# Optimization experiments

Hardware: AMD Instinct MI355X
Metric: run time of the kernel (lower is better)

The kernel has to match this reference:

```python
import jax, jax.numpy as jnp
import numpy as np

SR = 24000          # sample_rate
HOP = 256           # hop_length
K = 1024            # FIR kernel_size = nearest_power_of_two(2.2/50*24000)
RC = 512            # rnn_channels
NF = 4              # n_formants
REV = 24000         # reverb length in samples
L = HOP + K - 1     # per-frame conv output length = 1279
PI = np.pi


def _gru(x, W_ih, W_hh, b_ih, b_hh):
    # x: [B, T, H] -> [B, T, H], torch nn.GRU semantics, h0 = 0
    B = x.shape[0]

    def step(h, xt):
        gi = xt @ W_ih.T + b_ih
        gh = h @ W_hh.T + b_hh
        i_r, i_z, i_n = jnp.split(gi, 3, axis=-1)
        h_r, h_z, h_n = jnp.split(gh, 3, axis=-1)
        r = jax.nn.sigmoid(i_r + h_r)
        zg = jax.nn.sigmoid(i_z + h_z)
        n = jnp.tanh(i_n + r * h_n)
        h = (1.0 - zg) * n + zg * h
        return h, h

    h0 = jnp.zeros((B, RC), x.dtype)
    _, ys = jax.lax.scan(step, h0, jnp.swapaxes(x, 0, 1))
    return jnp.swapaxes(ys, 0, 1)


def setup_inputs() -> dict:
    key = jax.random.key(0)
    ks = jax.random.split(key, 20)
    B, F = 4, 2048
    s = 0.05
    inp = {
        'f0': jax.random.uniform(ks[0], (B, F, 1), minval=100.0, maxval=300.0),
        'loudness': jax.random.normal(ks[1], (B, F, 1)),
        'gender': jax.random.uniform(ks[2], (B, F, 2)),
        'age': jax.random.uniform(ks[3], (B, F, 8)),
        'z': jax.random.normal(ks[4], (B, F, 16)),
        'noise': jax.random.normal(ks[5], (B, F, HOP)),
        'W_in': jax.random.normal(ks[6], (RC, 28)) * s, 'b_in': jnp.zeros((RC,)),
        'W_ih': jax.random.normal(ks[7], (3 * RC, RC)) * s,
        'W_hh': jax.random.normal(ks[8], (3 * RC, RC)) * s,
        'b_ih': jnp.zeros((3 * RC,)), 'b_hh': jnp.zeros((3 * RC,)),
        'W_oq': jax.random.normal(ks[9], (1, RC)) * s, 'b_oq': jnp.zeros((1,)),
        'W_vg': jax.random.normal(ks[10], (1, RC)) * s, 'b_vg': jnp.zeros((1,)),
        'W_ug': jax.random.normal(ks[11], (1, RC)) * s, 'b_ug': jnp.zeros((1,)),
        'W_ff': jax.random.normal(ks[12], (NF, RC)) * s, 'b_ff': jnp.zeros((NF,)),
        'W_fb': jax.random.normal(ks[13], (NF, RC)) * s, 'b_fb': jnp.zeros((NF,)),
        'reverb_ir': jax.random.normal(ks[14], (REV,)) * jnp.exp(-jnp.linspace(0.0, 5.0, REV)),
        'wet_logit': jnp.float32(-1.5),
    }
    return inp


def reference(f0, loudness, gender, age, z, noise,
              W_in, b_in, W_ih, W_hh, b_ih, b_hh,
              W_oq, b_oq, W_vg, b_vg, W_ug, b_ug,
              W_ff, b_ff, W_fb, b_fb, reverb_ir, wet_logit):
    B, F, _ = f0.shape

    # ---- controller ----
    f0c = f0 - jnp.mean(f0, axis=1, keepdims=True)
    inputs = jnp.concatenate([f0c, loudness, gender, age, z], axis=-1)  # [B,F,28]
    x = jax.nn.relu(inputs @ W_in.T + b_in)
    x = _gru(x, W_ih, W_hh, b_ih, b_hh)                                  # [B,F,512]
    oq = jax.nn.sigmoid(x @ W_oq.T + b_oq)                               # [B,F,1]
    v_gain = jax.nn.softplus(x @ W_vg.T + b_vg)
    u_gain = jax.nn.softplus(x @ W_ug.T + b_ug)
    ff = jnp.cumsum(jax.nn.softplus(x @ W_ff.T + b_ff), axis=-1) + 200.0  # [B,F,4]
    fb = jax.nn.softplus(x @ W_fb.T + b_fb) + 50.0

    # ---- Rosenberg glottal source ----
    cycles = f0 * (HOP / SR)                       # [B,F,1]
    cum = jnp.cumsum(cycles, axis=1)
    start = cum - cycles
    start = start - jnp.floor(start)
    ramp = (jnp.arange(HOP, dtype=f0.dtype) / SR)[None, None, :]
    total = start + f0 * ramp                      # [B,F,HOP]
    phi = total - jnp.floor(total)
    eps = 1e-6
    peak = oq * 0.66
    rise = 0.5 * (1.0 - jnp.cos(PI * phi / (peak + eps)))
    fall = jnp.cos(PI * (phi - peak) / (2.0 * (oq - peak) + eps))
    voiced = jnp.where(phi < peak, rise, 0.0)
    voiced = jnp.where((phi >= peak) & (phi < oq), fall, voiced)

    # ---- excitation ----
    excitation = voiced * v_gain + noise * u_gain   # [B,F,HOP]

    # ---- time-varying FIR formant filter ----
    t = jnp.arange(K, dtype=f0.dtype) / SR          # [K]
    ir = jnp.exp(-PI * fb[..., None] * t) * jnp.sin(2.0 * PI * ff[..., None] * t)  # [B,F,4,K]
    combined = jnp.sum(ir, axis=2)                  # [B,F,K]
    scale = jnp.max(jnp.abs(combined), axis=-1, keepdims=True) + 1e-8
    filt = combined / scale
    # torch conv1d is cross-correlation with padding K-1 == full convolution with flipped kernel
    NFFT = 2048  # >= L = 1279, power of two
    Xf = jnp.fft.rfft(excitation, n=NFFT)
    Hf = jnp.fft.rfft(filt[..., ::-1], n=NFFT)
    conv = jnp.fft.irfft(Xf * Hf, n=NFFT)[..., :L]  # [B,F,L]

    # ---- overlap-add (F.fold) ----
    total_len = (F - 1) * HOP + L
    idx = (jnp.arange(F)[:, None] * HOP + jnp.arange(L)[None, :]).reshape(-1)
    audio = jnp.zeros((B, total_len), conv.dtype).at[:, idx].add(conv.reshape(B, -1))

    # ---- FFT reverb ----
    FFTN = 1 << 20  # >= total_len + REV - 1 = 549310
    Af = jnp.fft.rfft(audio, n=FFTN)
    Rf = jnp.fft.rfft(reverb_ir, n=FFTN)
    wetsig = jnp.fft.irfft(Af * Rf[None, :], n=FFTN)[:, :total_len]
    wet = jax.nn.sigmoid(wet_logit)
    out = ((1.0 - wet) * audio + wet * wetsig)[..., None]  # [B,total_len,1]

    return out, oq, v_gain, u_gain, ff, fb
```

## Files before the change

kernel.cpp:

```cpp
#include <hip/hip_runtime.h>
#include <hip/hip_bf16.h>
#include <math.h>

#define PI_F 3.14159265358979323846f
#define TWO_PI_F 6.283185307179586f

constexpr int BB = 4;
constexpr int FF_ = 2048;
constexpr int RC = 512;
constexpr int HOP = 256;
constexpr int KK = 1024;
constexpr int LL = HOP + KK - 1;
constexpr size_t TOT = 525311;
constexpr int APAD = 24064;
constexpr size_t AROW = 549376;
constexpr int REV = 24000;
constexpr size_t AROW2 = 551424;

constexpr size_t O1 = 2101244;
constexpr size_t O2 = 2109436;
constexpr size_t O3 = 2117628;
constexpr size_t O4 = 2125820;
constexpr size_t O5 = 2158588;

constexpr size_t OFF_X      = 0;
constexpr size_t OFF_GI     = 16777216;
constexpr size_t OFF_HS     = 67108864;
constexpr size_t OFF_OQ     = 83886080;
constexpr size_t OFF_VG     = 83918848;
constexpr size_t OFF_UG     = 83951616;
constexpr size_t OFF_FFW    = 83984384;
constexpr size_t OFF_FBW    = 84115456;
constexpr size_t OFF_START  = 84246528;
constexpr size_t OFF_F0M    = 84279296;
constexpr size_t OFF_WTAP   = 50331648;
constexpr size_t OFF_AUDIO  = 92684800;
constexpr size_t OFF_AF16   = OFF_X;

constexpr size_t OFF_HBUF   = OFF_FFW;

__device__ __forceinline__ float softplusf(float x) {
  return x > 20.0f ? x : log1pf(expf(x));
}
__device__ __forceinline__ float sigmoidf_(float x) {
  return 1.0f / (1.0f + expf(-x));
}
__device__ __forceinline__ float fastrcp(float x) {
#if __has_builtin(__builtin_amdgcn_rcpf)
  return __builtin_amdgcn_rcpf(x);
#else
  return 1.0f / x;
#endif
}

typedef _Float16 half2v __attribute__((ext_vector_type(2)));
typedef _Float16 f16x8 __attribute__((ext_vector_type(8)));
typedef float f32x4 __attribute__((ext_vector_type(4)));

__device__ __forceinline__ float dot2f(unsigned wa, unsigned hb, float acc) {
#if __has_builtin(__builtin_amdgcn_fdot2)
  union { unsigned u; half2v h; } A, B;
  A.u = wa; B.u = hb;
  return __builtin_amdgcn_fdot2(A.h, B.h, acc, false);
#else
  union { unsigned u; _Float16 h[2]; } A, B;
  A.u = wa; B.u = hb;
  return fmaf((float)A.h[0], (float)B.h[0], fmaf((float)A.h[1], (float)B.h[1], acc));
#endif
}

__global__ __launch_bounds__(256) void k_f0mean(const float* __restrict__ f0, float* __restrict__ f0m) {
  int b = blockIdx.x, tid = threadIdx.x;
  float s = 0.f;
  for (int t = tid; t < FF_; t += 256) s += f0[b*FF_ + t];
  #pragma unroll
  for (int m = 1; m < 64; m <<= 1) s += __shfl_xor(s, m);
  __shared__ float ws4[4];
  if ((tid & 63) == 0) ws4[tid >> 6] = s;
  __syncthreads();
  if (tid == 0) f0m[b] = (ws4[0] + ws4[1] + ws4[2] + ws4[3]) * (1.0f / 2048.0f);
}

__global__ __launch_bounds__(256) void k_inproj(
    const float* __restrict__ f0, const float* __restrict__ loud,
    const float* __restrict__ gender, const float* __restrict__ age,
    const float* __restrict__ z, const float* __restrict__ f0m,
    const float* __restrict__ Win, const float* __restrict__ bin,
    float* __restrict__ x)
{
  __shared__ float inp[16 * 28];
  int r0 = blockIdx.x * 16;
  int tid = threadIdx.x;
  for (int i = tid; i < 16 * 28; i += 256) {
    int r = i / 28, c = i % 28;
    int bf = r0 + r, b = bf >> 11;
    float v;
    if (c == 0)       v = f0[bf] - f0m[b];
    else if (c == 1)  v = loud[bf];
    else if (c < 4)   v = gender[(size_t)bf*2 + (c - 2)];
    else if (c < 12)  v = age[(size_t)bf*8 + (c - 4)];
    else              v = z[(size_t)bf*16 + (c - 12)];
    inp[i] = v;
  }
  __syncthreads();
  for (int o = tid; o < 16 * 512; o += 256) {
    int r = o >> 9, j = o & 511;
    const float* w = Win + j * 28;
    const float* ip = inp + r * 28;
    float a = bin[j];
    #pragma unroll
    for (int c2 = 0; c2 < 28; ++c2) a = fmaf(w[c2], ip[c2], a);
    x[(size_t)(r0 + r) * 512 + j] = fmaxf(a, 0.0f);
  }
}

__global__ __launch_bounds__(256) void k_gemm_gi(
    const float* __restrict__ A, const float* __restrict__ Bw,
    const float* __restrict__ bias, float* __restrict__ C)
{
  __shared__ unsigned As[64 * 20];
  __shared__ unsigned Bs[64 * 20];
  int tid = threadIdx.x;
  int n0 = blockIdx.x * 64, m0 = blockIdx.y * 64;
  const int w = tid >> 6;
  const int lane = tid & 63;
  const int mrow0 = (w >> 1) * 32;
  const int ncol0 = (w & 1) * 32;
  const int lm = lane & 15;
  const int quad = lane >> 4;

  f32x4 acc00 = {0.f,0.f,0.f,0.f}, acc01 = {0.f,0.f,0.f,0.f};
  f32x4 acc10 = {0.f,0.f,0.f,0.f}, acc11 = {0.f,0.f,0.f,0.f};

  for (int k0 = 0; k0 < 512; k0 += 32) {
    __syncthreads();
    for (int i = tid; i < 1024; i += 256) {
      int r = i >> 4, d = i & 15;
      float2 av = *(const float2*)(A + (size_t)(m0 + r) * 512 + k0 + 2 * d);
      float2 bv = *(const float2*)(Bw + (size_t)(n0 + r) * 512 + k0 + 2 * d);
      union { unsigned u32; _Float16 h[2]; } pa, pb;
      pa.h[0] = (_Float16)av.x; pa.h[1] = (_Float16)av.y;
      pb.h[0] = (_Float16)bv.x; pb.h[1] = (_Float16)bv.y;
      As[r * 20 + d] = pa.u32;
      Bs[r * 20 + d] = pb.u32;
    }
    __syncthreads();
    union { uint4 u; f16x8 h; } a0, a1, b0, b1;
    a0.u = *(const uint4*)&As[(mrow0 + lm) * 20 + quad * 4];
    a1.u = *(const uint4*)&As[(mrow0 + 16 + lm) * 20 + quad * 4];
    b0.u = *(const uint4*)&Bs[(ncol0 + lm) * 20 + quad * 4];
    b1.u = *(const uint4*)&Bs[(ncol0 + 16 + lm) * 20 + quad * 4];
    acc00 = __builtin_amdgcn_mfma_f32_16x16x32_f16(a0.h, b0.h, acc00, 0, 0, 0);
    acc01 = __builtin_amdgcn_mfma_f32_16x16x32_f16(a0.h, b1.h, acc01, 0, 0, 0);
    acc10 = __builtin_amdgcn_mfma_f32_16x16x32_f16(a1.h, b0.h, acc10, 0, 0, 0);
    acc11 = __builtin_amdgcn_mfma_f32_16x16x32_f16(a1.h, b1.h, acc11, 0, 0, 0);
  }
  #pragma unroll
  for (int sm = 0; sm < 2; ++sm) {
    #pragma unroll
    for (int sn = 0; sn < 2; ++sn) {
      const f32x4& ac = sm ? (sn ? acc11 : acc10) : (sn ? acc01 : acc00);
      int col = n0 + ncol0 + sn * 16 + lm;
      float bb = bias[col];
      #pragma unroll
      for (int rg = 0; rg < 4; ++rg) {
        int row = m0 + mrow0 + sm * 16 + quad * 4 + rg;
        C[(size_t)row * 1536 + col] = ac[rg] + bb;
      }
    }
  }
}

__global__ __launch_bounds__(256, 1) void k_gru(
    const float* __restrict__ Whh, const float* __restrict__ bhh,
    const float* __restrict__ gi, float* __restrict__ hs,
    unsigned long long* hbuf)
{
  __shared__ unsigned hs2[2][292];
  __shared__ float red[2][384];
  __shared__ float bhh_s[96];

  const int tid = threadIdx.x;
  const int bid = blockIdx.x;
  const int b   = (bid & 7) >> 1;
  const int wgi = ((bid >> 3) << 1) | (bid & 1);
  const int u0  = wgi * 32;
  const int piece = tid & 3;
  const int rp    = tid >> 2;

  unsigned w0r[64], w1r[64];
  if (tid < 192) {
    int r0 = 2 * rp, r1 = 2 * rp + 1;
    const float* s0 = Whh + (size_t)((r0 >> 5) * 512 + u0 + (r0 & 31)) * 512 + piece * 128;
    const float* s1 = Whh + (size_t)((r1 >> 5) * 512 + u0 + (r1 & 31)) * 512 + piece * 128;
    #pragma unroll
    for (int j = 0; j < 64; ++j) {
      float2 a = *(const float2*)(s0 + 2 * j);
      float2 c = *(const float2*)(s1 + 2 * j);
      union { unsigned u32; _Float16 hh[2]; } ca, cb;
      ca.hh[0] = (_Float16)a.x; ca.hh[1] = (_Float16)a.y;
      cb.hh[0] = (_Float16)c.x; cb.hh[1] = (_Float16)c.y;
      w0r[j] = ca.u32; w1r[j] = cb.u32;
    }
  } else {
    #pragma unroll
    for (int j = 0; j < 64; ++j) { w0r[j] = 0u; w1r[j] = 0u; }
  }
  if (tid < 96) bhh_s[tid] = bhh[(tid >> 5) * 512 + u0 + (tid & 31)];
  __syncthreads();

  float hprev = 0.0f;

  #pragma unroll 1
  for (unsigned t = 0; t < 2048; ++t) {
    const int p = (int)(t & 1u);
    float gir = 0.f, giz = 0.f, gin = 0.f;
    if (tid < 32) {
      const float* gp = gi + (size_t)(b * 2048 + (int)t) * 1536 + u0 + tid;
      gir = gp[0]; giz = gp[512]; gin = gp[1024];
    }
    {
      const unsigned long long* pp = hbuf + ((size_t)p * 4 + b) * 256 + tid;
      unsigned long long w = __hip_atomic_load(pp, __ATOMIC_RELAXED, __HIP_MEMORY_SCOPE_AGENT);
      while ((unsigned)(w >> 32) != t)
        w = __hip_atomic_load(pp, __ATOMIC_RELAXED, __HIP_MEMORY_SCOPE_AGENT);
      hs2[p][(tid >> 5) * 36 + (tid & 31)] = (unsigned)w;
    }
    __syncthreads();
    if (tid < 192) {
      const unsigned* hp0 = &hs2[p][(2 * piece) * 36];
      const unsigned* hp1 = &hs2[p][(2 * piece + 1) * 36];
      float a00 = 0.f, a01 = 0.f, a10 = 0.f, a11 = 0.f;
      #pragma unroll
      for (int i = 0; i < 8; ++i) {
        uint4 h4 = *(const uint4*)(hp0 + 4 * i);
        a00 = dot2f(w0r[4 * i + 0], h4.x, a00);
        a01 = dot2f(w0r[4 * i + 1], h4.y, a01);
        a00 = dot2f(w0r[4 * i + 2], h4.z, a00);
        a01 = dot2f(w0r[4 * i + 3], h4.w, a01);
        a10 = dot2f(w1r[4 * i + 0], h4.x, a10);
        a11 = dot2f(w1r[4 * i + 1], h4.y, a11);
        a10 = dot2f(w1r[4 * i + 2], h4.z, a10);
        a11 = dot2f(w1r[4 * i + 3], h4.w, a11);
      }
      #pragma unroll
      for (int i = 0; i < 8; ++i) {
        uint4 h4 = *(const uint4*)(hp1 + 4 * i);
        a00 = dot2f(w0r[32 + 4 * i + 0], h4.x, a00);
        a01 = dot2f(w0r[32 + 4 * i + 1], h4.y, a01);
        a00 = dot2f(w0r[32 + 4 * i + 2], h4.z, a00);
        a01 = dot2f(w0r[32 + 4 * i + 3], h4.w, a01);
        a10 = dot2f(w1r[32 + 4 * i + 0], h4.x, a10);
        a11 = dot2f(w1r[32 + 4 * i + 1], h4.y, a11);
        a10 = dot2f(w1r[32 + 4 * i + 2], h4.z, a10);
        a11 = dot2f(w1r[32 + 4 * i + 3], h4.w, a11);
      }
      red[p][(2 * rp) * 4 + piece]     = a00 + a01;
      red[p][(2 * rp + 1) * 4 + piece] = a10 + a11;
    }
    __syncthreads();
    if (tid < 32) {
      float4 q0 = *(const float4*)&red[p][tid * 4];
      float4 z0 = *(const float4*)&red[p][(32 + tid) * 4];
      float4 n0 = *(const float4*)&red[p][(64 + tid) * 4];
      float ghr = ((q0.x + q0.y) + (q0.z + q0.w)) + bhh_s[tid];
      float ghz = ((z0.x + z0.y) + (z0.z + z0.w)) + bhh_s[32 + tid];
      float ghn = ((n0.x + n0.y) + (n0.z + n0.w)) + bhh_s[64 + tid];
      float r  = fastrcp(1.0f + __expf(-(gir + ghr)));
      float zg = fastrcp(1.0f + __expf(-(giz + ghz)));
      float e2 = __expf(2.0f * (gin + r * ghn));
      float n  = 1.0f - 2.0f * fastrcp(e2 + 1.0f);
      float hnew = (1.0f - zg) * n + zg * hprev;
      hprev = hnew;
      float hpart = __shfl_xor(hnew, 1);
      if ((tid & 1) == 0) {
        union { unsigned u32; _Float16 hh[2]; } pk;
        pk.hh[0] = (_Float16)hnew;
        pk.hh[1] = (_Float16)hpart;
        unsigned long long wq = ((unsigned long long)(t + 1u) << 32) | (unsigned long long)pk.u32;
        __hip_atomic_store(hbuf + ((size_t)((t + 1u) & 1u) * 4 + b) * 256 + (u0 >> 1) + (tid >> 1),
                           wq, __ATOMIC_RELAXED, __HIP_MEMORY_SCOPE_AGENT);
      }
      hs[(size_t)(b * 2048 + (int)t) * 512 + u0 + tid] = hnew;
    }
  }
}

__global__ __launch_bounds__(256) void k_heads(
    const float* __restrict__ hs,
    const float* __restrict__ Woq, const float* __restrict__ boq,
    const float* __restrict__ Wvg, const float* __restrict__ bvg,
    const float* __restrict__ Wug, const float* __restrict__ bug,
    const float* __restrict__ Wff, const float* __restrict__ bff,
    const float* __restrict__ Wfb, const float* __restrict__ bfb,
    float* __restrict__ out,
    float* __restrict__ oqw, float* __restrict__ vgw, float* __restrict__ ugw,
    float* __restrict__ ffw, float* __restrict__ fbw)
{
  int bf = blockIdx.x, tid = threadIdx.x;
  const float* h = hs + (size_t)bf * 512;
  float p[11];
  #pragma unroll
  for (int i = 0; i < 11; ++i) p[i] = 0.f;
  for (int k = tid; k < 512; k += 256) {
    float hv = h[k];
    p[0] = fmaf(Woq[k], hv, p[0]);
    p[1] = fmaf(Wvg[k], hv, p[1]);
    p[2] = fmaf(Wug[k], hv, p[2]);
    p[3] = fmaf(Wff[k], hv, p[3]);
    p[4] = fmaf(Wff[512 + k], hv, p[4]);
    p[5] = fmaf(Wff[1024 + k], hv, p[5]);
    p[6] = fmaf(Wff[1536 + k], hv, p[6]);
    p[7] = fmaf(Wfb[k], hv, p[7]);
    p[8] = fmaf(Wfb[512 + k], hv, p[8]);
    p[9] = fmaf(Wfb[1024 + k], hv, p[9]);
    p[10] = fmaf(Wfb[1536 + k], hv, p[10]);
  }
  #pragma unroll
  for (int i = 0; i < 11; ++i) {
    float v = p[i];
    #pragma unroll
    for (int m = 1; m < 64; m <<= 1) v += __shfl_xor(v, m);
    p[i] = v;
  }
  __shared__ float r4[4][11];
  if ((tid & 63) == 0) {
    int w = tid >> 6;
    #pragma unroll
    for (int i = 0; i < 11; ++i) r4[w][i] = p[i];
  }
  __syncthreads();
  if (tid == 0) {
    float s[11];
    #pragma unroll
    for (int i = 0; i < 11; ++i) s[i] = r4[0][i] + r4[1][i] + r4[2][i] + r4[3][i];
    float oqv = sigmoidf_(s[0] + boq[0]);
    float vg = softplusf(s[1] + bvg[0]);
    float ug = softplusf(s[2] + bug[0]);
    out[O1 + bf] = oqv; oqw[bf] = oqv;
    out[O2 + bf] = vg;  vgw[bf] = vg;
    out[O3 + bf] = ug;  ugw[bf] = ug;
    float run = 200.0f;
    #pragma unroll
    for (int j = 0; j < 4; ++j) {
      run += softplusf(s[3 + j] + bff[j]);
      out[O4 + (size_t)bf * 4 + j] = run; ffw[(size_t)bf * 4 + j] = run;
    }
    #pragma unroll
    for (int j = 0; j < 4; ++j) {
      float g = softplusf(s[7 + j] + bfb[j]) + 50.0f;
      out[O5 + (size_t)bf * 4 + j] = g; fbw[(size_t)bf * 4 + j] = g;
    }
  }
}

__global__ __launch_bounds__(256) void k_scan(const float* __restrict__ f0, float* __restrict__ startw) {
  __shared__ float ts[256];
  int b = blockIdx.x, tid = threadIdx.x;
  const float CY = 256.0f / 24000.0f;
  float c[8], run = 0.f;
  int base = b * 2048 + tid * 8;
  #pragma unroll
  for (int j = 0; j < 8; ++j) { c[j] = run; run += f0[base + j] * CY; }
  ts[tid] = run;
  __syncthreads();
  for (int off = 1; off < 256; off <<= 1) {
    float v = (tid >= off) ? ts[tid - off] : 0.0f;
    __syncthreads();
    ts[tid] += v;
    __syncthreads();
  }
  float excl = (tid == 0) ? 0.0f : ts[tid - 1];
  #pragma unroll
  for (int j = 0; j < 8; ++j) {
    float st = excl + c[j];
    startw[base + j] = st - floorf(st);
  }
}

__global__ __launch_bounds__(256) void k_synth(
    const float* __restrict__ f0, const float* __restrict__ noise,
    const float* __restrict__ startw, const float* __restrict__ oqw,
    const float* __restrict__ vgw, const float* __restrict__ ugw,
    const float* __restrict__ ffw, const float* __restrict__ fbw,
    float* __restrict__ audio)
{
  __shared__ float es[256];
  __shared__ float fp[1536];
  __shared__ float ffs[4], fbs[4], ssc[1], wmax[4];
  int bf = blockIdx.x, tid = threadIdx.x;
  int b = bf >> 11, f = bf & 2047;

  {
    float st = startw[bf], f0v = f0[bf], oqv = oqw[bf], vg = vgw[bf], ug = ugw[bf];
    float total = st + f0v * ((float)tid * (1.0f / 24000.0f));
    float phi = total - floorf(total);
    float peak = oqv * 0.66f;
    float rise = 0.5f * (1.0f - __cosf(PI_F * phi / (peak + 1e-6f)));
    float fall = __cosf(PI_F * (phi - peak) / (2.0f * (oqv - peak) + 1e-6f));
    float v = (phi < peak) ? rise : ((phi < oqv) ? fall : 0.0f);
    es[tid] = v * vg + noise[(size_t)bf * 256 + tid] * ug;
  }
  if (tid < 4) { ffs[tid] = ffw[(size_t)bf * 4 + tid]; fbs[tid] = fbw[(size_t)bf * 4 + tid]; }
  fp[tid] = 0.0f;
  fp[1280 + tid] = 0.0f;
  __syncthreads();

  float vals[4];
  float am = 0.f;
  #pragma unroll
  for (int it = 0; it < 4; ++it) {
    int k = it * 256 + tid;
    float t = (float)k * (1.0f / 24000.0f);
    float s = 0.f;
    #pragma unroll
    for (int j = 0; j < 4; ++j)
      s += __expf(-PI_F * fbs[j] * t) * __sinf(TWO_PI_F * ffs[j] * t);
    vals[it] = s;
    am = fmaxf(am, fabsf(s));
  }
  #pragma unroll
  for (int m = 1; m < 64; m <<= 1) am = fmaxf(am, __shfl_xor(am, m));
  if ((tid & 63) == 0) wmax[tid >> 6] = am;
  __syncthreads();
  if (tid == 0) ssc[0] = fmaxf(fmaxf(wmax[0], wmax[1]), fmaxf(wmax[2], wmax[3])) + 1e-8f;
  __syncthreads();
  float inv = 1.0f / ssc[0];
  #pragma unroll
  for (int it = 0; it < 4; ++it) {
    int k = it * 256 + tid;
    fp[256 + (1023 - k)] = vals[it] * inv;
  }
  __syncthreads();

  int n0 = tid * 5;
  float V0 = fp[n0 + 256], V1 = fp[n0 + 257], V2 = fp[n0 + 258], V3 = fp[n0 + 259], V4 = fp[n0 + 260];
  float a0 = 0.f, a1 = 0.f, a2 = 0.f, a3 = 0.f, a4 = 0.f;
  #pragma unroll 4
  for (int m = 0; m < 256; ++m) {
    float e = es[m];
    a0 = fmaf(e, V0, a0); a1 = fmaf(e, V1, a1); a2 = fmaf(e, V2, a2);
    a3 = fmaf(e, V3, a3); a4 = fmaf(e, V4, a4);
    V4 = V3; V3 = V2; V2 = V1; V1 = V0;
    V0 = fp[n0 + 255 - m];
  }
  float* arow = audio + (size_t)b * AROW + APAD + (size_t)f * 256;
  if (n0 + 0 < LL) atomicAdd(&arow[n0 + 0], a0);
  if (n0 + 1 < LL) atomicAdd(&arow[n0 + 1], a1);
  if (n0 + 2 < LL) atomicAdd(&arow[n0 + 2], a2);
  if (n0 + 3 < LL) atomicAdd(&arow[n0 + 3], a3);
  if (n0 + 4 < LL) atomicAdd(&arow[n0 + 4], a4);
}

__global__ __launch_bounds__(256) void k_packaudio(const float* __restrict__ audio,
                                                   unsigned* __restrict__ af) {
  int idx = blockIdx.x * 256 + threadIdx.x;
  int b = blockIdx.y;
  size_t i0 = (size_t)idx * 2;
  if (i0 < AROW2) {
    float a = (i0 < AROW)     ? audio[(size_t)b * AROW + i0]     : 0.0f;
    float c = (i0 + 1 < AROW) ? audio[(size_t)b * AROW + i0 + 1] : 0.0f;
    union { unsigned u32; _Float16 h[2]; } pk;
    pk.h[0] = (_Float16)a; pk.h[1] = (_Float16)c;
    af[(size_t)b * (AROW2 / 2) + idx] = pk.u32;
  }
}

__global__ __launch_bounds__(256) void k_wtaps(const float* __restrict__ ir, uint4* __restrict__ wtap) {
  int g = blockIdx.x * 256 + threadIdx.x;
  int p = g >> 6, l = g & 63;
  if (p < 752) {
    int base = 32 * p + 16 + (l & 15) - ((l >> 4) << 3);
    unsigned dw[4];
    #pragma unroll
    for (int j = 0; j < 4; ++j) {
      int i0 = base - 2 * j, i1 = base - 2 * j - 1;
      float v0 = (i0 >= 0 && i0 < REV) ? ir[i0] : 0.0f;
      float v1 = (i1 >= 0 && i1 < REV) ? ir[i1] : 0.0f;
      union { unsigned u32; _Float16 h[2]; } pk;
      pk.h[0] = (_Float16)v0; pk.h[1] = (_Float16)v1;
      dw[j] = pk.u32;
    }
    uint4 o; o.x = dw[0]; o.y = dw[1]; o.z = dw[2]; o.w = dw[3];
    wtap[(size_t)(p << 6) + l] = o;
  }
}

constexpr int PC = 16;
constexpr int NCHUNK = 47;
constexpr int WINH = 2544;

__global__ __launch_bounds__(256) void k_reverb(
    const float* __restrict__ audio, const unsigned short* __restrict__ af,
    const uint4* __restrict__ wtap, const float* __restrict__ wetl,
    float* __restrict__ out)
{
  __shared__ __align__(16) unsigned short win[WINH];
  __shared__ uint4 wlds[PC * 64];
  int tb = blockIdx.x, b = blockIdx.y, tid = threadIdx.x;
  const int wv = tid >> 6, lane = tid & 63;
  const int lm = lane & 15, quad = lane >> 4;
  int q0 = tb * 128;
  const unsigned short* afrow = af + (size_t)b * AROW2;
  f32x4 acc0 = {0.f,0.f,0.f,0.f}, acc1 = {0.f,0.f,0.f,0.f};

  for (int c = 0; c < NCHUNK; ++c) {
    int p0 = c * PC;
    int b_lo = 16 * q0 - 32 * (p0 + PC - 1) - 16;
    const uint4* src = (const uint4*)(afrow + (APAD + b_lo));
    __syncthreads();
    for (int u = tid; u < 318 + PC * 64; u += 256) {
      if (u < 318) ((uint4*)win)[u] = src[u];
      else         wlds[u - 318] = wtap[(size_t)p0 * 64 + (u - 318)];
    }
    __syncthreads();
    int offb = 16 * lm + 8 * quad;
    int tA = (2 * wv) * 256 + offb, tB = (2 * wv + 1) * 256 + offb;
    #pragma unroll 4
    for (int pl = 0; pl < PC; ++pl) {
      union { uint4 u; f16x8 h; } wf, b0, b1;
      wf.u = wlds[pl * 64 + lane];
      int offp = 32 * (PC - 1 - pl);
      b0.u = *(const uint4*)&win[offp + tA];
      b1.u = *(const uint4*)&win[offp + tB];
      acc0 = __builtin_amdgcn_mfma_f32_16x16x32_f16(wf.h, b0.h, acc0, 0, 0, 0);
      acc1 = __builtin_amdgcn_mfma_f32_16x16x32_f16(wf.h, b1.h, acc1, 0, 0, 0);
    }
  }
  float wet = sigmoidf_(wetl[0]);
  const float* arow = audio + (size_t)b * AROW;
  #pragma unroll
  for (int tile = 0; tile < 2; ++tile) {
    const f32x4& ac = tile ? acc1 : acc0;
    int qt = q0 + (2 * wv + tile) * 16 + lm;
    #pragma unroll
    for (int rg = 0; rg < 4; ++rg) {
      long t = (long)16 * qt + quad * 4 + rg;
      if (t < (long)TOT) {
        float av = arow[APAD + t];
        out[(size_t)b * TOT + t] = (1.0f - wet) * av + wet * ac[rg];
      }
    }
  }
}

extern "C" void kernel_launch(void* const* d_in, const int* in_sizes, int n_in,
                              void* d_out, int out_size, void* d_ws, size_t ws_size,
                              hipStream_t stream) {
  const float* f0       = (const float*)d_in[0];
  const float* loud     = (const float*)d_in[1];
  const float* gender   = (const float*)d_in[2];
  const float* age      = (const float*)d_in[3];
  const float* z        = (const float*)d_in[4];
  const float* noise    = (const float*)d_in[5];
  const float* W_in     = (const float*)d_in[6];
  const float* b_in     = (const float*)d_in[7];
  const float* W_ih     = (const float*)d_in[8];
  const float* W_hh     = (const float*)d_in[9];
  const float* b_ih     = (const float*)d_in[10];
  const float* b_hh     = (const float*)d_in[11];
  const float* W_oq     = (const float*)d_in[12];
  const float* b_oq     = (const float*)d_in[13];
  const float* W_vg     = (const float*)d_in[14];
  const float* b_vg     = (const float*)d_in[15];
  const float* W_ug     = (const float*)d_in[16];
  const float* b_ug     = (const float*)d_in[17];
  const float* W_ff     = (const float*)d_in[18];
  const float* b_ff     = (const float*)d_in[19];
  const float* W_fb     = (const float*)d_in[20];
  const float* b_fb     = (const float*)d_in[21];
  const float* rev_ir   = (const float*)d_in[22];
  const float* wet_l    = (const float*)d_in[23];

  float* out = (float*)d_out;
  char* ws = (char*)d_ws;
  float* x      = (float*)(ws + OFF_X);
  float* gi     = (float*)(ws + OFF_GI);
  float* hs     = (float*)(ws + OFF_HS);
  float* oqw    = (float*)(ws + OFF_OQ);
  float* vgw    = (float*)(ws + OFF_VG);
  float* ugw    = (float*)(ws + OFF_UG);
  float* ffw    = (float*)(ws + OFF_FFW);
  float* fbw    = (float*)(ws + OFF_FBW);
  float* startw = (float*)(ws + OFF_START);
  float* f0m    = (float*)(ws + OFF_F0M);
  unsigned long long* hbuf = (unsigned long long*)(ws + OFF_HBUF);
  uint4* wtap   = (uint4*)(ws + OFF_WTAP);
  unsigned* af  = (unsigned*)(ws + OFF_AF16);
  float* audio  = (float*)(ws + OFF_AUDIO);

  hipMemsetAsync(ws + OFF_HBUF, 0, 16384, stream);
  hipMemsetAsync(ws + OFF_AUDIO, 0, (size_t)4 * AROW * 4, stream);

  k_f0mean<<<4, 256, 0, stream>>>(f0, f0m);
  k_inproj<<<512, 256, 0, stream>>>(f0, loud, gender, age, z, f0m, W_in, b_in, x);
  k_gemm_gi<<<dim3(24, 128), 256, 0, stream>>>(x, W_ih, b_ih, gi);
  k_gru<<<64, 256, 0, stream>>>(W_hh, b_hh, gi, hs, hbuf);
  k_heads<<<8192, 256, 0, stream>>>(hs, W_oq, b_oq, W_vg, b_vg, W_ug, b_ug,
                                    W_ff, b_ff, W_fb, b_fb, out, oqw, vgw, ugw, ffw, fbw);
  k_scan<<<4, 256, 0, stream>>>(f0, startw);
  k_wtaps<<<188, 256, 0, stream>>>(rev_ir, wtap);
  k_synth<<<8192, 256, 0, stream>>>(f0, noise, startw, oqw, vgw, ugw, ffw, fbw, audio);
  k_packaudio<<<dim3(1077, 4), 256, 0, stream>>>(audio, af);
  k_reverb<<<dim3(257, 4), 256, 0, stream>>>(audio, (const unsigned short*)af, wtap, wet_l, out);
}
```

Baseline: 3.237 ms.

## Fuse output heads into persistent GRU kernel using idle warp

Removes the separate k_heads kernel and the hs store. The fourth warp of each GRU block, which sat idle before, now holds fp16 head weights in registers and computes all 11 head projections for one frame out of every 16, rotated across blocks. It runs off the shared hidden state from the previous step, and the loop gains one extra iteration so the last frame is covered. Head math switches to fp16 dot products and fast exp/log, which could slightly change accuracy. The extra work sits inside the latency-bound recurrent loop and could lengthen its critical path.

```diff
diff --git a/kernel.cpp b/kernel.cpp
--- a/kernel.cpp
+++ b/kernel.cpp
@@ -25,7 +25,6 @@
 
 constexpr size_t OFF_X      = 0;
 constexpr size_t OFF_GI     = 16777216;
-constexpr size_t OFF_HS     = 67108864;
 constexpr size_t OFF_OQ     = 83886080;
 constexpr size_t OFF_VG     = 83918848;
 constexpr size_t OFF_UG     = 83951616;
@@ -33,11 +32,10 @@
 constexpr size_t OFF_FBW    = 84115456;
 constexpr size_t OFF_START  = 84246528;
 constexpr size_t OFF_F0M    = 84279296;
+constexpr size_t OFF_HBUF   = 84283392;
 constexpr size_t OFF_WTAP   = 50331648;
 constexpr size_t OFF_AUDIO  = 92684800;
 constexpr size_t OFF_AF16   = OFF_X;
-
-constexpr size_t OFF_HBUF   = OFF_FFW;
 
 __device__ __forceinline__ float softplusf(float x) {
   return x > 20.0f ? x : log1pf(expf(x));
@@ -51,6 +49,9 @@
 #else
   return 1.0f / x;
 #endif
+}
+__device__ __forceinline__ float fastsoftplus(float x) {
+  return x > 20.0f ? x : __logf(1.0f + __expf(x));
 }
 
 typedef _Float16 half2v __attribute__((ext_vector_type(2)));
@@ -173,8 +174,15 @@
 
 __global__ __launch_bounds__(256, 1) void k_gru(
     const float* __restrict__ Whh, const float* __restrict__ bhh,
-    const float* __restrict__ gi, float* __restrict__ hs,
-    unsigned long long* hbuf)
+    const float* __restrict__ gi, unsigned long long* hbuf,
+    const float* __restrict__ Woq, const float* __restrict__ boq,
+    const float* __restrict__ Wvg, const float* __restrict__ bvg,
+    const float* __restrict__ Wug, const float* __restrict__ bug,
+    const float* __restrict__ Wff, const float* __restrict__ bff,
+    const float* __restrict__ Wfb, const float* __restrict__ bfb,
+    float* __restrict__ out,
+    float* __restrict__ oqw, float* __restrict__ vgw, float* __restrict__ ugw,
+    float* __restrict__ ffw, float* __restrict__ fbw)
 {
   __shared__ unsigned hs2[2][292];
   __shared__ float red[2][384];
@@ -189,6 +197,9 @@
   const int rp    = tid >> 2;
 
   unsigned w0r[64], w1r[64];
+  float hb0 = 0.f, hb1 = 0.f, hb2 = 0.f;
+  float hbf0 = 0.f, hbf1 = 0.f, hbf2 = 0.f, hbf3 = 0.f;
+  float hbb0 = 0.f, hbb1 = 0.f, hbb2 = 0.f, hbb3 = 0.f;
   if (tid < 192) {
     int r0 = 2 * rp, r1 = 2 * rp + 1;
     const float* s0 = Whh + (size_t)((r0 >> 5) * 512 + u0 + (r0 & 31)) * 512 + piece * 128;
@@ -203,8 +214,28 @@
       w0r[j] = ca.u32; w1r[j] = cb.u32;
     }
   } else {
+    int j = tid - 192;
     #pragma unroll
-    for (int j = 0; j < 64; ++j) { w0r[j] = 0u; w1r[j] = 0u; }
+    for (int q = 0; q < 64; ++q) { w0r[q] = 0u; w1r[q] = 0u; }
+    if (j < 44) {
+      int hd = j >> 2, pc = j & 3;
+      const float* rowp = (hd == 0) ? Woq : (hd == 1) ? Wvg : (hd == 2) ? Wug :
+                          (hd < 7) ? (Wff + (size_t)(hd - 3) * 512)
+                                   : (Wfb + (size_t)(hd - 7) * 512);
+      const float* srcw = rowp + pc * 128;
+      #pragma unroll
+      for (int q = 0; q < 64; ++q) {
+        float2 a = *(const float2*)(srcw + 2 * q);
+        union { unsigned u32; _Float16 hh[2]; } ca;
+        ca.hh[0] = (_Float16)a.x; ca.hh[1] = (_Float16)a.y;
+        w0r[q] = ca.u32;
+      }
+    }
+    if (j == 0) {
+      hb0 = boq[0]; hb1 = bvg[0]; hb2 = bug[0];
+      hbf0 = bff[0]; hbf1 = bff[1]; hbf2 = bff[2]; hbf3 = bff[3];
+      hbb0 = bfb[0]; hbb1 = bfb[1]; hbb2 = bfb[2]; hbb3 = bfb[3];
+    }
   }
   if (tid < 96) bhh_s[tid] = bhh[(tid >> 5) * 512 + u0 + (tid & 31)];
   __syncthreads();
@@ -212,10 +243,10 @@
   float hprev = 0.0f;
 
   #pragma unroll 1
-  for (unsigned t = 0; t < 2048; ++t) {
+  for (unsigned t = 0; t <= 2048; ++t) {
     const int p = (int)(t & 1u);
     float gir = 0.f, giz = 0.f, gin = 0.f;
-    if (tid < 32) {
+    if (tid < 32 && t < 2048u) {
       const float* gp = gi + (size_t)(b * 2048 + (int)t) * 1536 + u0 + tid;
       gir = gp[0]; giz = gp[512]; gin = gp[1024];
     }
@@ -227,7 +258,7 @@
       hs2[p][(tid >> 5) * 36 + (tid & 31)] = (unsigned)w;
     }
     __syncthreads();
-    if (tid < 192) {
+    if (tid < 192 && t < 2048u) {
       const unsigned* hp0 = &hs2[p][(2 * piece) * 36];
       const unsigned* hp1 = &hs2[p][(2 * piece + 1) * 36];
       float a00 = 0.f, a01 = 0.f, a10 = 0.f, a11 = 0.f;
@@ -258,8 +289,57 @@
       red[p][(2 * rp) * 4 + piece]     = a00 + a01;
       red[p][(2 * rp + 1) * 4 + piece] = a10 + a11;
     }
-    __syncthreads();
-    if (tid < 32) {
+    if (tid >= 192 && t >= 1u && (int)((t - 1u) & 15u) == wgi) {
+      unsigned fr = t - 1u;
+      int j = tid - 192;
+      int pc = j & 3;
+      const unsigned* hh0 = &hs2[p][(2 * pc) * 36];
+      const unsigned* hh1 = &hs2[p][(2 * pc + 1) * 36];
+      float a0 = 0.f, a1 = 0.f;
+      #pragma unroll
+      for (int i = 0; i < 8; ++i) {
+        uint4 h4 = *(const uint4*)(hh0 + 4 * i);
+        a0 = dot2f(w0r[4 * i + 0], h4.x, a0);
+        a1 = dot2f(w0r[4 * i + 1], h4.y, a1);
+        a0 = dot2f(w0r[4 * i + 2], h4.z, a0);
+        a1 = dot2f(w0r[4 * i + 3], h4.w, a1);
+      }
+      #pragma unroll
+      for (int i = 0; i < 8; ++i) {
+        uint4 h4 = *(const uint4*)(hh1 + 4 * i);
+        a0 = dot2f(w0r[32 + 4 * i + 0], h4.x, a0);
+        a1 = dot2f(w0r[32 + 4 * i + 1], h4.y, a1);
+        a0 = dot2f(w0r[32 + 4 * i + 2], h4.z, a0);
+        a1 = dot2f(w0r[32 + 4 * i + 3], h4.w, a1);
+      }
+      float vs = a0 + a1;
+      vs += __shfl_xor(vs, 1);
+      vs += __shfl_xor(vs, 2);
+      float s0 = __shfl(vs, 0),  s1 = __shfl(vs, 4),  s2 = __shfl(vs, 8);
+      float s3 = __shfl(vs, 12), s4 = __shfl(vs, 16), s5 = __shfl(vs, 20);
+      float s6 = __shfl(vs, 24), s7 = __shfl(vs, 28), s8 = __shfl(vs, 32);
+      float s9 = __shfl(vs, 36), s10 = __shfl(vs, 40);
+      if (j == 0) {
+        size_t bf = (size_t)b * 2048 + fr;
+        float oqv = fastrcp(1.0f + __expf(-(s0 + hb0)));
+        float vg = fastsoftplus(s1 + hb1);
+        float ug = fastsoftplus(s2 + hb2);
+        out[O1 + bf] = oqv; oqw[bf] = oqv;
+        out[O2 + bf] = vg;  vgw[bf] = vg;
+        out[O3 + bf] = ug;  ugw[bf] = ug;
+        float run = 200.0f;
+        run += fastsoftplus(s3 + hbf0); out[O4 + bf * 4 + 0] = run; ffw[bf * 4 + 0] = run;
+        run += fastsoftplus(s4 + hbf1); out[O4 + bf * 4 + 1] = run; ffw[bf * 4 + 1] = run;
+        run += fastsoftplus(s5 + hbf2); out[O4 + bf * 4 + 2] = run; ffw[bf * 4 + 2] = run;
+        run += fastsoftplus(s6 + hbf3); out[O4 + bf * 4 + 3] = run; ffw[bf * 4 + 3] = run;
+        float g0 = fastsoftplus(s7 + hbb0) + 50.0f;  out[O5 + bf * 4 + 0] = g0; fbw[bf * 4 + 0] = g0;
+        float g1 = fastsoftplus(s8 + hbb1) + 50.0f;  out[O5 + bf * 4 + 1] = g1; fbw[bf * 4 + 1] = g1;
+        float g2 = fastsoftplus(s9 + hbb2) + 50.0f;  out[O5 + bf * 4 + 2] = g2; fbw[bf * 4 + 2] = g2;
+        float g3 = fastsoftplus(s10 + hbb3) + 50.0f; out[O5 + bf * 4 + 3] = g3; fbw[bf * 4 + 3] = g3;
+      }
+    }
+    __syncthreads();
+    if (tid < 32 && t < 2048u) {
       float4 q0 = *(const float4*)&red[p][tid * 4];
       float4 z0 = *(const float4*)&red[p][(32 + tid) * 4];
       float4 n0 = *(const float4*)&red[p][(64 + tid) * 4];
@@ -281,75 +361,6 @@
         __hip_atomic_store(hbuf + ((size_t)((t + 1u) & 1u) * 4 + b) * 256 + (u0 >> 1) + (tid >> 1),
                            wq, __ATOMIC_RELAXED, __HIP_MEMORY_SCOPE_AGENT);
       }
-      hs[(size_t)(b * 2048 + (int)t) * 512 + u0 + tid] = hnew;
-    }
-  }
-}
-
-__global__ __launch_bounds__(256) void k_heads(
-    const float* __restrict__ hs,
-    const float* __restrict__ Woq, const float* __restrict__ boq,
-    const float* __restrict__ Wvg, const float* __restrict__ bvg,
-    const float* __restrict__ Wug, const float* __restrict__ bug,
-    const float* __restrict__ Wff, const float* __restrict__ bff,
-    const float* __restrict__ Wfb, const float* __restrict__ bfb,
-    float* __restrict__ out,
-    float* __restrict__ oqw, float* __restrict__ vgw, float* __restrict__ ugw,
-    float* __restrict__ ffw, float* __restrict__ fbw)
-{
-  int bf = blockIdx.x, tid = threadIdx.x;
-  const float* h = hs + (size_t)bf * 512;
-  float p[11];
-  #pragma unroll
-  for (int i = 0; i < 11; ++i) p[i] = 0.f;
-  for (int k = tid; k < 512; k += 256) {
-    float hv = h[k];
-    p[0] = fmaf(Woq[k], hv, p[0]);
-    p[1] = fmaf(Wvg[k], hv, p[1]);
-    p[2] = fmaf(Wug[k], hv, p[2]);
-    p[3] = fmaf(Wff[k], hv, p[3]);
-    p[4] = fmaf(Wff[512 + k], hv, p[4]);
-    p[5] = fmaf(Wff[1024 + k], hv, p[5]);
-    p[6] = fmaf(Wff[1536 + k], hv, p[6]);
-    p[7] = fmaf(Wfb[k], hv, p[7]);
-    p[8] = fmaf(Wfb[512 + k], hv, p[8]);
-    p[9] = fmaf(Wfb[1024 + k], hv, p[9]);
-    p[10] = fmaf(Wfb[1536 + k], hv, p[10]);
-  }
-  #pragma unroll
-  for (int i = 0; i < 11; ++i) {
-    float v = p[i];
-    #pragma unroll
-    for (int m = 1; m < 64; m <<= 1) v += __shfl_xor(v, m);
-    p[i] = v;
-  }
-  __shared__ float r4[4][11];
-  if ((tid & 63) == 0) {
-    int w = tid >> 6;
-    #pragma unroll
-    for (int i = 0; i < 11; ++i) r4[w][i] = p[i];
-  }
-  __syncthreads();
-  if (tid == 0) {
-    float s[11];
-    #pragma unroll
-    for (int i = 0; i < 11; ++i) s[i] = r4[0][i] + r4[1][i] + r4[2][i] + r4[3][i];
-    float oqv = sigmoidf_(s[0] + boq[0]);
-    float vg = softplusf(s[1] + bvg[0]);
-    float ug = softplusf(s[2] + bug[0]);
-    out[O1 + bf] = oqv; oqw[bf] = oqv;
-    out[O2 + bf] = vg;  vgw[bf] = vg;
-    out[O3 + bf] = ug;  ugw[bf] = ug;
-    float run = 200.0f;
-    #pragma unroll
-    for (int j = 0; j < 4; ++j) {
-      run += softplusf(s[3 + j] + bff[j]);
-      out[O4 + (size_t)bf * 4 + j] = run; ffw[(size_t)bf * 4 + j] = run;
-    }
-    #pragma unroll
-    for (int j = 0; j < 4; ++j) {
-      float g = softplusf(s[7 + j] + bfb[j]) + 50.0f;
-      out[O5 + (size_t)bf * 4 + j] = g; fbw[(size_t)bf * 4 + j] = g;
     }
   }
 }
@@ -576,7 +587,6 @@
   char* ws = (char*)d_ws;
   float* x      = (float*)(ws + OFF_X);
   float* gi     = (float*)(ws + OFF_GI);
-  float* hs     = (float*)(ws + OFF_HS);
   float* oqw    = (float*)(ws + OFF_OQ);
   float* vgw    = (float*)(ws + OFF_VG);
   float* ugw    = (float*)(ws + OFF_UG);
@@ -595,9 +605,10 @@
   k_f0mean<<<4, 256, 0, stream>>>(f0, f0m);
   k_inproj<<<512, 256, 0, stream>>>(f0, loud, gender, age, z, f0m, W_in, b_in, x);
   k_gemm_gi<<<dim3(24, 128), 256, 0, stream>>>(x, W_ih, b_ih, gi);
-  k_gru<<<64, 256, 0, stream>>>(W_hh, b_hh, gi, hs, hbuf);
-  k_heads<<<8192, 256, 0, stream>>>(hs, W_oq, b_oq, W_vg, b_vg, W_ug, b_ug,
-                                    W_ff, b_ff, W_fb, b_fb, out, oqw, vgw, ugw, ffw, fbw);
+  k_gru<<<64, 256, 0, stream>>>(W_hh, b_hh, gi, hbuf,
+                                W_oq, b_oq, W_vg, b_vg, W_ug, b_ug,
+                                W_ff, b_ff, W_fb, b_fb,
+                                out, oqw, vgw, ugw, ffw, fbw);
   k_scan<<<4, 256, 0, stream>>>(f0, startw);
   k_wtaps<<<188, 256, 0, stream>>>(rev_ir, wtap);
   k_synth<<<8192, 256, 0, stream>>>(f0, noise, startw, oqw, vgw, ugw, ffw, fbw, audio);
```

Result: slower. 3.897 ms (+20.4%).
